# Kernel optimization log

Measured on AMD Instinct MI355X. Metric: run time of the kernel, lower is better.

Reference implementation:

```python
import jax, jax.numpy as jnp
import numpy as np
from jax.ops import segment_sum, segment_max

N, E, F, H, G, P, C = 50000, 600000, 128, 128, 64, 32, 10
HEADS = 3
BN_EPS = 1e-5
COS_EPS = 1e-8


def setup_inputs() -> dict:
    key = jax.random.key(0)
    ks = jax.random.split(key, 32)
    rn = lambda k, shape, s: jax.random.normal(k, shape, jnp.float32) * s
    inp = {
        "x": jax.random.normal(ks[0], (N, F), jnp.float32),
        "edge_index": jax.random.randint(ks[1], (2, E), 0, N, jnp.int32),
        "batch": jnp.sort(jax.random.randint(ks[2], (N,), 0, G, jnp.int32)),
        # GCNConv
        "W1": rn(ks[3], (F, H), F ** -0.5), "b1": jnp.zeros((H,), jnp.float32),
        # SAGEConv (lin_l on aggregated neighbors, lin_r on root)
        "Wl": rn(ks[4], (H, H), H ** -0.5), "Wr": rn(ks[5], (H, H), H ** -0.5),
        "bs": jnp.zeros((H,), jnp.float32),
        # GATConv, heads=3, concat=False
        "Wg": rn(ks[6], (H, HEADS * H), H ** -0.5),
        "a_src": rn(ks[7], (HEADS, H), H ** -0.5),
        "a_dst": rn(ks[8], (HEADS, H), H ** -0.5),
        "bg": jnp.zeros((H,), jnp.float32),
        # prototype head / classifier / decoder
        "protos": jax.random.normal(ks[9], (P, H), jnp.float32),
        "Wc": rn(ks[10], (H, C), H ** -0.5), "bc": jnp.zeros((C,), jnp.float32),
        "Wd1": rn(ks[11], (H, 2 * H), H ** -0.5), "bd1": jnp.zeros((2 * H,), jnp.float32),
        "Wd2": rn(ks[12], (2 * H, F), (2 * H) ** -0.5), "bd2": jnp.zeros((F,), jnp.float32),
    }
    # BatchNorm (eval mode): gamma, beta, running mean/var for bn1..bn3
    for i in range(3):
        k0, k1, k2 = jax.random.split(ks[13 + i], 3)
        inp[f"g{i+1}"] = 1.0 + rn(k0, (H,), 0.05)
        inp[f"be{i+1}"] = rn(k1, (H,), 0.05)
        inp[f"m{i+1}"] = rn(k2, (H,), 0.1)
        inp[f"v{i+1}"] = jnp.ones((H,), jnp.float32)
    return inp


def _bn(x, g, b, m, v):
    return (x - m) * jax.lax.rsqrt(v + BN_EPS) * g + b


def _forward(x, edge_index, batch,
             W1, b1, g1, be1, m1, v1,
             Wl, Wr, bs, g2, be2, m2, v2,
             Wg, a_src, a_dst, bg, g3, be3, m3, v3,
             protos, Wc, bc, Wd1, bd1, Wd2, bd2):
    src, dst = edge_index[0], edge_index[1]
    ones_e = jnp.ones((src.shape[0],), x.dtype)

    # --- GCNConv: symmetric norm with self-loops ---
    h = x @ W1                                        # [N, H]
    deg = segment_sum(ones_e, dst, num_segments=N) + 1.0
    dinv = jax.lax.rsqrt(deg)
    coef = dinv[src] * dinv[dst]                      # [E]
    h1 = segment_sum(h[src] * coef[:, None], dst, num_segments=N)
    h1 = h1 + h * (dinv * dinv)[:, None] + b1         # self-loop term + bias
    h1 = jax.nn.elu(_bn(h1, g1, be1, m1, v1))         # dropout = identity (eval)

    # --- SAGEConv: mean aggregation (no self-loops) ---
    cnt = segment_sum(ones_e, dst, num_segments=N)
    mean_nb = segment_sum(h1[src], dst, num_segments=N) / jnp.maximum(cnt, 1.0)[:, None]
    h2 = mean_nb @ Wl + h1 @ Wr + bs
    h2 = jax.nn.elu(_bn(h2, g2, be2, m2, v2))

    # --- GATConv: heads=3, concat=False (mean), with self-loops ---
    hg = (h2 @ Wg).reshape(N, HEADS, H)               # [N, 3, H]
    al_src = jnp.einsum('nhf,hf->nh', hg, a_src)      # [N, 3]
    al_dst = jnp.einsum('nhf,hf->nh', hg, a_dst)
    loop = jnp.arange(N, dtype=src.dtype)
    s2 = jnp.concatenate([src, loop])
    d2 = jnp.concatenate([dst, loop])
    e = jax.nn.leaky_relu(al_src[s2] + al_dst[d2], 0.2)   # [E+N, 3]
    emax = segment_max(e, d2, num_segments=N)             # every node has a self-loop
    ex = jnp.exp(e - emax[d2])
    den = segment_sum(ex, d2, num_segments=N)
    alpha = ex / den[d2]                                  # [E+N, 3]
    h3 = segment_sum(hg[s2] * alpha[:, :, None], d2, num_segments=N)
    h3 = h3.mean(axis=1) + bg                             # concat=False -> head mean
    h3 = jax.nn.elu(_bn(h3, g3, be3, m3, v3))

    # --- global mean pool over graphs ---
    gcnt = segment_sum(jnp.ones((N,), x.dtype), batch, num_segments=G)
    pooled = segment_sum(h3, batch, num_segments=G) / jnp.maximum(gcnt, 1.0)[:, None]

    # --- prototype head: cosine sim -> softmax -> mix ---
    xn = pooled / jnp.maximum(jnp.linalg.norm(pooled, axis=-1, keepdims=True), COS_EPS)
    pn = protos / jnp.maximum(jnp.linalg.norm(protos, axis=-1, keepdims=True), COS_EPS)
    sims = xn @ pn.T                                      # [G, P]
    assignments = jax.nn.softmax(sims, axis=-1)
    proto_emb = assignments @ protos                      # [G, H]
    logits = proto_emb @ Wc + bc                          # [G, C]
    reconstructed = jax.nn.relu(pooled @ Wd1 + bd1) @ Wd2 + bd2   # [G, F]
    return logits, proto_emb, assignments, reconstructed


def reference(x, edge_index, batch,
              W1, b1, g1, be1, m1, v1,
              Wl, Wr, bs, g2, be2, m2, v2,
              Wg, a_src, a_dst, bg, g3, be3, m3, v3,
              protos, Wc, bc, Wd1, bd1, Wd2, bd2):
    return _forward(x, edge_index, batch,
                    W1, b1, g1, be1, m1, v1,
                    Wl, Wr, bs, g2, be2, m2, v2,
                    Wg, a_src, a_dst, bg, g3, be3, m3, v3,
                    protos, Wc, bc, Wd1, bd1, Wd2, bd2)
```

## Files before the change

### kernel.cpp

```cpp
#include <hip/hip_runtime.h>
#include <hip/hip_bf16.h>
#include <stdint.h>
#include <stddef.h>

#define N_ 50000
#define E_ 600000
#define F_ 128
#define H_ 128
#define G_ 64
#define P_ 32
#define C_ 10
#define NB_ 49

typedef __hip_bfloat16 bf16;
typedef __attribute__((ext_vector_type(8))) short short8;
typedef __attribute__((ext_vector_type(4))) float float4v;

struct __align__(4) u3 { unsigned int x, y, z; };

__device__ __forceinline__ float b2f(bf16 x){ return __bfloat162float(x); }
__device__ __forceinline__ float us2f(unsigned short u){ return __uint_as_float(((unsigned int)u)<<16); }
__device__ __forceinline__ unsigned short f2us(float x){ bf16 h = __float2bfloat16(x); return *(unsigned short*)&h; }
__device__ __forceinline__ float blo(unsigned int u){ return __uint_as_float(u<<16); }
__device__ __forceinline__ float bhi(unsigned int u){ return __uint_as_float(u & 0xFFFF0000u); }
__device__ __forceinline__ float eluf(float x){ return x>0.f ? x : expm1f(x); }
__device__ __forceinline__ float bnf(float x,float m,float v,float g,float b){ return (x-m)*rsqrtf(v+1e-5f)*g+b; }
__device__ __forceinline__ float lrelu(float x){ return x>0.f ? x : 0.2f*x; }
__device__ __forceinline__ float expc(float x){ return __expf(fminf(x, 50.f)); }
__device__ __forceinline__ void atomAddF(float* a, float v){ unsafeAtomicAdd(a, v); }

__global__ __launch_bounds__(256) void k_wprep(const float* __restrict__ W1, const float* __restrict__ Wl,
    const float* __restrict__ Wr, const float* __restrict__ Wg, unsigned short* __restrict__ WT){
  int idx = blockIdx.x*256 + threadIdx.x;
  if(idx >= 6*16384) return;
  int m = idx >> 14, rem = idx & 16383;
  int n = rem >> 7, k = rem & 127;
  float v;
  if(m==0)      v = W1[k*128+n];
  else if(m==1) v = Wl[k*128+n];
  else if(m==2) v = Wr[k*128+n];
  else          v = Wg[k*384 + (m-3)*128 + n];
  WT[idx] = f2us(v);
}

__device__ __forceinline__ void stage_WT(const unsigned short* __restrict__ WTg, unsigned short* lds, int tid){
  #pragma unroll
  for(int i=0;i<8;i++){
    int idx = tid + i*256;
    int n = idx>>4, c = idx&15;
    uint4 v = *(const uint4*)(WTg + (size_t)idx*8);
    int cs = c ^ (n & 15);
    *(uint4*)(lds + n*128 + cs*8) = v;
  }
}
__device__ __forceinline__ short8 read_Bfrag(const unsigned short* lds, int tile, int kc, int lane){
  int n = tile*16 + (lane&15);
  int c = kc*4 + (lane>>4);
  int cs = c ^ (lane & 15);
  return *(const short8*)(lds + n*128 + cs*8);
}
__device__ __forceinline__ void load_Afrag_bf16(const bf16* A, int row, int lane, short8 af[4]){
  const unsigned short* ap = (const unsigned short*)A + (size_t)row*128 + (lane>>4)*8;
  #pragma unroll
  for(int kc=0;kc<4;kc++) af[kc] = *(const short8*)(ap + kc*32);
}
__device__ __forceinline__ void mfma_pass(const unsigned short* lds, const short8 af[4], int lane, float4v acc[8]){
  #pragma unroll
  for(int tile=0;tile<8;tile++){
    #pragma unroll
    for(int kc=0;kc<4;kc++){
      short8 bfv = read_Bfrag(lds, tile, kc, lane);
      acc[tile] = __builtin_amdgcn_mfma_f32_16x16x32_bf16(af[kc], bfv, acc[tile], 0, 0, 0);
    }
  }
}

__global__ __launch_bounds__(256) void k_mm_x(const float* __restrict__ X, const unsigned short* __restrict__ WTg,
                                              bf16* __restrict__ HB){
  __shared__ unsigned short Wlds[128*128];
  const int tid = threadIdx.x, lane = tid&63, w = tid>>6;
  const int row0 = blockIdx.x*64;
  stage_WT(WTg, Wlds, tid);
  int arow = row0 + w*16 + (lane&15);
  int ar = arow < N_ ? arow : N_-1;
  const float* ap = X + (size_t)ar*128 + (lane>>4)*8;
  short8 af[4];
  #pragma unroll
  for(int kc=0;kc<4;kc++){
    float4 a = *(const float4*)(ap + kc*32);
    float4 b = *(const float4*)(ap + kc*32 + 4);
    short8 v;
    v[0]=(short)f2us(a.x); v[1]=(short)f2us(a.y); v[2]=(short)f2us(a.z); v[3]=(short)f2us(a.w);
    v[4]=(short)f2us(b.x); v[5]=(short)f2us(b.y); v[6]=(short)f2us(b.z); v[7]=(short)f2us(b.w);
    af[kc]=v;
  }
  __syncthreads();
  float4v acc[8];
  #pragma unroll
  for(int t=0;t<8;t++){ acc[t][0]=0.f; acc[t][1]=0.f; acc[t][2]=0.f; acc[t][3]=0.f; }
  mfma_pass(Wlds, af, lane, acc);
  const int colb = lane&15, q = lane>>4;
  unsigned short* ob = (unsigned short*)HB;
  #pragma unroll
  for(int r=0;r<4;r++){
    int ro = row0 + w*16 + q*4 + r;
    if(ro < N_){
      #pragma unroll
      for(int tile=0;tile<8;tile++)
        ob[(size_t)ro*128 + tile*16 + colb] = f2us(acc[tile][r]);
    }
  }
}

__global__ __launch_bounds__(256) void k_sage_mm(const bf16* __restrict__ MaB, const bf16* __restrict__ H1B,
    const unsigned short* __restrict__ WlT, const unsigned short* __restrict__ WrT,
    const float* __restrict__ bs, const float* __restrict__ g2, const float* __restrict__ be2,
    const float* __restrict__ m2, const float* __restrict__ v2, bf16* __restrict__ H2B){
  __shared__ unsigned short Wlds[128*128];
  const int tid = threadIdx.x, lane = tid&63, w = tid>>6;
  const int row0 = blockIdx.x*64;
  int arow = row0 + w*16 + (lane&15);
  int ar = arow < N_ ? arow : N_-1;
  float4v acc[8];
  #pragma unroll
  for(int t=0;t<8;t++){ acc[t][0]=0.f; acc[t][1]=0.f; acc[t][2]=0.f; acc[t][3]=0.f; }
  short8 af[4];

  stage_WT(WlT, Wlds, tid);
  load_Afrag_bf16(MaB, ar, lane, af);
  __syncthreads();
  mfma_pass(Wlds, af, lane, acc);
  __syncthreads();
  stage_WT(WrT, Wlds, tid);
  load_Afrag_bf16(H1B, ar, lane, af);
  __syncthreads();
  mfma_pass(Wlds, af, lane, acc);

  const int colb = lane&15, q = lane>>4;
  unsigned short* ob = (unsigned short*)H2B;
  #pragma unroll
  for(int tile=0;tile<8;tile++){
    int col = tile*16 + colb;
    float bsv=bs[col], gv=g2[col], bev=be2[col], mv=m2[col], vv=v2[col];
    #pragma unroll
    for(int r=0;r<4;r++){
      int ro = row0 + w*16 + q*4 + r;
      if(ro < N_){
        float x = acc[tile][r] + bsv;
        ob[(size_t)ro*128 + col] = f2us(eluf(bnf(x, mv, vv, gv, bev)));
      }
    }
  }
}

__global__ __launch_bounds__(256) void k_gat_mm_all(const bf16* __restrict__ H2B, const unsigned short* __restrict__ WgT,
    const float* __restrict__ a_src, const float* __restrict__ a_dst,
    bf16* __restrict__ HG3I, float* __restrict__ als3, float* __restrict__ ald3){
  __shared__ unsigned short Wlds[128*128];
  const int tid = threadIdx.x, lane = tid&63, w = tid>>6;
  const int row0 = blockIdx.x*64;
  int arow = row0 + w*16 + (lane&15);
  int ar = arow < N_ ? arow : N_-1;
  short8 af[4];
  load_Afrag_bf16(H2B, ar, lane, af);
  const int colb = lane&15, q = lane>>4;
  unsigned short* ob = (unsigned short*)HG3I;
  for(int hh=0; hh<3; hh++){
    if(hh) __syncthreads();
    stage_WT(WgT + hh*16384, Wlds, tid);
    __syncthreads();
    float4v acc[8];
    #pragma unroll
    for(int t=0;t<8;t++){ acc[t][0]=0.f; acc[t][1]=0.f; acc[t][2]=0.f; acc[t][3]=0.f; }
    mfma_pass(Wlds, af, lane, acc);
    float asv[8], adv[8];
    #pragma unroll
    for(int tile=0;tile<8;tile++){
      asv[tile] = a_src[hh*128 + tile*16 + colb];
      adv[tile] = a_dst[hh*128 + tile*16 + colb];
    }
    #pragma unroll
    for(int r=0;r<4;r++){
      int ro = row0 + w*16 + q*4 + r;
      float ps = 0.f, pd = 0.f;
      #pragma unroll
      for(int tile=0;tile<8;tile++){ ps += acc[tile][r]*asv[tile]; pd += acc[tile][r]*adv[tile]; }
      #pragma unroll
      for(int o=8;o>0;o>>=1){ ps += __shfl_down(ps,o,16); pd += __shfl_down(pd,o,16); }
      if(ro < N_){
        #pragma unroll
        for(int tile=0;tile<8;tile++)
          ob[(size_t)ro*384 + (size_t)(tile*8 + (colb>>1))*6 + hh*2 + (colb&1)] = f2us(acc[tile][r]);
        if(colb == 0){ als3[ro*3+hh] = ps; ald3[ro*3+hh] = pd; }
      }
    }
  }
}

__global__ __launch_bounds__(256) void k_count(const int* __restrict__ dst, int* __restrict__ cnt){
  int e = blockIdx.x*256 + threadIdx.x;
  if(e < E_) atomicAdd(&cnt[dst[e]], 1);
}

__global__ __launch_bounds__(1024) void k_scan1(const int* __restrict__ cnt, int* __restrict__ row_ptr,
                                                float* __restrict__ dinv, int* __restrict__ bsum){
  __shared__ int wsum[16];
  const int t = threadIdx.x, lane = t & 63, wid = t >> 6;
  int i = blockIdx.x*1024 + t;
  int v = (i<N_) ? cnt[i] : 0;
  int x = v;
  #pragma unroll
  for(int o=1;o<64;o<<=1){
    int y = __shfl_up(x, o, 64);
    if(lane >= o) x += y;
  }
  if(lane==63) wsum[wid] = x;
  __syncthreads();
  if(wid==0){
    int s = (lane<16) ? wsum[lane] : 0;
    #pragma unroll
    for(int o=1;o<16;o<<=1){
      int y = __shfl_up(s, o, 64);
      if(lane >= o) s += y;
    }
    if(lane<16) wsum[lane] = s;
  }
  __syncthreads();
  int waveoff = (wid>0) ? wsum[wid-1] : 0;
  int incl = waveoff + x;
  if(i<N_){
    row_ptr[i] = incl - v;
    dinv[i] = rsqrtf((float)v + 1.f);
  }
  if(t==1023) bsum[blockIdx.x] = incl;
}

__global__ __launch_bounds__(64) void k_scan2(const int* __restrict__ bsum, int* __restrict__ boff,
                                              int* __restrict__ row_ptr){
  int lane = threadIdx.x;
  int v = (lane < NB_) ? bsum[lane] : 0;
  int x = v;
  #pragma unroll
  for(int o=1;o<64;o<<=1){
    int y = __shfl_up(x, o, 64);
    if(lane >= o) x += y;
  }
  if(lane < NB_) boff[lane] = x - v;
  if(lane == 63) row_ptr[N_] = x;
}

__global__ __launch_bounds__(256) void k_scan3(int* __restrict__ row_ptr, const int* __restrict__ boff,
                                               int* __restrict__ tmp){
  int i = blockIdx.x*256 + threadIdx.x;
  if(i < N_){
    int r = row_ptr[i] + boff[i>>10];
    row_ptr[i] = r;
    tmp[i] = r;
  }
}

__global__ __launch_bounds__(256) void k_scatter(const int* __restrict__ src, const int* __restrict__ dst,
                                                 int* __restrict__ tmp, int* __restrict__ esrc,
                                                 int* __restrict__ edst){
  int e = blockIdx.x*256 + threadIdx.x;
  if(e < E_){
    int d = dst[e];
    int pos = atomicAdd(&tmp[d], 1);
    esrc[pos] = src[e];
    edst[pos] = d;
  }
}

__global__ __launch_bounds__(256) void k_wexp(const int* __restrict__ esrc, const int* __restrict__ edst,
    const float* __restrict__ als3, const float* __restrict__ ald3, float* __restrict__ we4){
  int e = blockIdx.x*256 + threadIdx.x;
  if(e >= E_) return;
  int s = esrc[e], d = edst[e];
  float4 w;
  w.x = expc(lrelu(als3[s*3+0] + ald3[d*3+0]));
  w.y = expc(lrelu(als3[s*3+1] + ald3[d*3+1]));
  w.z = expc(lrelu(als3[s*3+2] + ald3[d*3+2]));
  w.w = 0.f;
  *(float4*)(we4 + (size_t)e*4) = w;
}

__global__ __launch_bounds__(256) void k_gcn_gather(const int* __restrict__ row_ptr, const int* __restrict__ esrc,
    const float* __restrict__ dinv, const bf16* __restrict__ HB,
    const float* __restrict__ b1, const float* __restrict__ g1, const float* __restrict__ be1,
    const float* __restrict__ m1, const float* __restrict__ v1, bf16* __restrict__ H1B){
  int n = blockIdx.x*4 + (threadIdx.x>>6);
  int lane = threadIdx.x & 63;
  if(n >= N_) return;
  int beg = row_ptr[n], end = row_ptr[n+1];
  float dn = dinv[n];
  float a0 = 0.f, a1 = 0.f;
  const unsigned short* hb = (const unsigned short*)HB;
  int e = beg;
  for(; e+3 < end; e += 4){
    int s0 = esrc[e], s1 = esrc[e+1], s2 = esrc[e+2], s3 = esrc[e+3];
    unsigned int hv0 = *(const unsigned int*)(hb + (size_t)s0*H_ + lane*2);
    unsigned int hv1 = *(const unsigned int*)(hb + (size_t)s1*H_ + lane*2);
    unsigned int hv2 = *(const unsigned int*)(hb + (size_t)s2*H_ + lane*2);
    unsigned int hv3 = *(const unsigned int*)(hb + (size_t)s3*H_ + lane*2);
    float c0 = dinv[s0]*dn, c1 = dinv[s1]*dn, c2 = dinv[s2]*dn, c3 = dinv[s3]*dn;
    a0 += c0*blo(hv0) + c1*blo(hv1) + c2*blo(hv2) + c3*blo(hv3);
    a1 += c0*bhi(hv0) + c1*bhi(hv1) + c2*bhi(hv2) + c3*bhi(hv3);
  }
  for(; e < end; e++){
    int s = esrc[e];
    float c = dinv[s]*dn;
    unsigned int hv = *(const unsigned int*)(hb + (size_t)s*H_ + lane*2);
    a0 += c*blo(hv);
    a1 += c*bhi(hv);
  }
  unsigned int hv = *(const unsigned int*)(hb + (size_t)n*H_ + lane*2);
  int f0 = lane*2, f1 = f0+1;
  float x0 = a0 + blo(hv)*dn*dn + b1[f0];
  float x1 = a1 + bhi(hv)*dn*dn + b1[f1];
  x0 = eluf(bnf(x0, m1[f0], v1[f0], g1[f0], be1[f0]));
  x1 = eluf(bnf(x1, m1[f1], v1[f1], g1[f1], be1[f1]));
  unsigned int o = ((unsigned int)f2us(x1)<<16) | f2us(x0);
  *(unsigned int*)((unsigned short*)H1B + (size_t)n*H_ + lane*2) = o;
}

__global__ __launch_bounds__(256) void k_sage_gather(const int* __restrict__ row_ptr, const int* __restrict__ esrc,
    const bf16* __restrict__ H1B, bf16* __restrict__ MeanB){
  int n = blockIdx.x*4 + (threadIdx.x>>6);
  int lane = threadIdx.x & 63;
  if(n >= N_) return;
  int beg = row_ptr[n], end = row_ptr[n+1];
  float a0 = 0.f, a1 = 0.f;
  const unsigned short* hb = (const unsigned short*)H1B;
  int e = beg;
  for(; e+3 < end; e += 4){
    int s0 = esrc[e], s1 = esrc[e+1], s2 = esrc[e+2], s3 = esrc[e+3];
    unsigned int hv0 = *(const unsigned int*)(hb + (size_t)s0*H_ + lane*2);
    unsigned int hv1 = *(const unsigned int*)(hb + (size_t)s1*H_ + lane*2);
    unsigned int hv2 = *(const unsigned int*)(hb + (size_t)s2*H_ + lane*2);
    unsigned int hv3 = *(const unsigned int*)(hb + (size_t)s3*H_ + lane*2);
    a0 += blo(hv0) + blo(hv1) + blo(hv2) + blo(hv3);
    a1 += bhi(hv0) + bhi(hv1) + bhi(hv2) + bhi(hv3);
  }
  for(; e < end; e++){
    unsigned int hv = *(const unsigned int*)(hb + (size_t)esrc[e]*H_ + lane*2);
    a0 += blo(hv);
    a1 += bhi(hv);
  }
  float inv = 1.f / fmaxf((float)(end-beg), 1.f);
  unsigned int o = ((unsigned int)f2us(a1*inv)<<16) | f2us(a0*inv);
  *(unsigned int*)((unsigned short*)MeanB + (size_t)n*H_ + lane*2) = o;
}

__global__ __launch_bounds__(256) void k_gat_gather3(const int* __restrict__ row_ptr, const int* __restrict__ esrc,
    const float* __restrict__ als3, const float* __restrict__ ald3, const float* __restrict__ we4,
    const bf16* __restrict__ HG3I, bf16* __restrict__ H3B){
  int n = blockIdx.x*4 + (threadIdx.x>>6);
  int lane = threadIdx.x & 63;
  if(n >= N_) return;
  int beg = row_ptr[n], end = row_ptr[n+1];
  float es0 = expc(lrelu(als3[n*3+0] + ald3[n*3+0]));
  float es1 = expc(lrelu(als3[n*3+1] + ald3[n*3+1]));
  float es2 = expc(lrelu(als3[n*3+2] + ald3[n*3+2]));
  const unsigned short* hb = (const unsigned short*)HG3I;
  const int lp6 = lane*6;
  u3 hs = *(const u3*)(hb + (size_t)n*384 + lp6);
  float den0 = es0, den1 = es1, den2 = es2;
  float a00 = es0*blo(hs.x), a01 = es0*bhi(hs.x);
  float a10 = es1*blo(hs.y), a11 = es1*bhi(hs.y);
  float a20 = es2*blo(hs.z), a21 = es2*bhi(hs.z);
  int e = beg;
  for(; e+3 < end; e += 4){
    int s0 = esrc[e], s1 = esrc[e+1], s2 = esrc[e+2], s3 = esrc[e+3];
    float4 w0 = *(const float4*)(we4 + (size_t)(e  )*4);
    float4 w1 = *(const float4*)(we4 + (size_t)(e+1)*4);
    float4 w2 = *(const float4*)(we4 + (size_t)(e+2)*4);
    float4 w3 = *(const float4*)(we4 + (size_t)(e+3)*4);
    u3 p0 = *(const u3*)(hb + (size_t)s0*384 + lp6);
    u3 p1 = *(const u3*)(hb + (size_t)s1*384 + lp6);
    u3 p2 = *(const u3*)(hb + (size_t)s2*384 + lp6);
    u3 p3 = *(const u3*)(hb + (size_t)s3*384 + lp6);
    den0 += w0.x + w1.x + w2.x + w3.x;
    den1 += w0.y + w1.y + w2.y + w3.y;
    den2 += w0.z + w1.z + w2.z + w3.z;
    a00 += w0.x*blo(p0.x) + w1.x*blo(p1.x) + w2.x*blo(p2.x) + w3.x*blo(p3.x);
    a01 += w0.x*bhi(p0.x) + w1.x*bhi(p1.x) + w2.x*bhi(p2.x) + w3.x*bhi(p3.x);
    a10 += w0.y*blo(p0.y) + w1.y*blo(p1.y) + w2.y*blo(p2.y) + w3.y*blo(p3.y);
    a11 += w0.y*bhi(p0.y) + w1.y*bhi(p1.y) + w2.y*bhi(p2.y) + w3.y*bhi(p3.y);
    a20 += w0.z*blo(p0.z) + w1.z*blo(p1.z) + w2.z*blo(p2.z) + w3.z*blo(p3.z);
    a21 += w0.z*bhi(p0.z) + w1.z*bhi(p1.z) + w2.z*bhi(p2.z) + w3.z*bhi(p3.z);
  }
  for(; e < end; e++){
    int s = esrc[e];
    float4 w = *(const float4*)(we4 + (size_t)e*4);
    u3 p = *(const u3*)(hb + (size_t)s*384 + lp6);
    den0 += w.x; den1 += w.y; den2 += w.z;
    a00 += w.x*blo(p.x); a01 += w.x*bhi(p.x);
    a10 += w.y*blo(p.y); a11 += w.y*bhi(p.y);
    a20 += w.z*blo(p.z); a21 += w.z*bhi(p.z);
  }
  float i0 = 1.f/(3.f*den0), i1 = 1.f/(3.f*den1), i2 = 1.f/(3.f*den2);
  float r0 = a00*i0 + a10*i1 + a20*i2;
  float r1 = a01*i0 + a11*i1 + a21*i2;
  unsigned int o = ((unsigned int)f2us(r1)<<16) | f2us(r0);
  *(unsigned int*)((unsigned short*)H3B + (size_t)n*H_ + lane*2) = o;
}

#define NPW_ 16
__global__ __launch_bounds__(256) void k_h3fin_pool(const bf16* __restrict__ ACCB, const float* __restrict__ bg,
    const float* __restrict__ g3, const float* __restrict__ be3, const float* __restrict__ m3, const float* __restrict__ v3,
    const int* __restrict__ batch, float* __restrict__ pooled, float* __restrict__ gcnt){
  int wave = blockIdx.x*4 + (threadIdx.x>>6);
  int lane = threadIdx.x & 63;
  int n0 = wave*NPW_;
  if(n0 >= N_) return;
  int n1 = n0 + NPW_; if(n1 > N_) n1 = N_;
  int f0 = lane*2, f1 = f0+1;
  float bg0=bg[f0], bg1=bg[f1];
  float g30=g3[f0], g31=g3[f1], be30=be3[f0], be31=be3[f1];
  float m30=m3[f0], m31=m3[f1], v30=v3[f0], v31=v3[f1];
  float r0=0.f, r1=0.f;
  int cur = batch[n0];
  int seg = 0;
  for(int n=n0; n<n1; n++){
    int b = batch[n];
    if(b != cur){
      atomAddF(&pooled[cur*H_ + f0], r0);
      atomAddF(&pooled[cur*H_ + f1], r1);
      if(lane==0) atomAddF(&gcnt[cur], (float)seg);
      r0 = 0.f; r1 = 0.f; seg = 0; cur = b;
    }
    unsigned int hv = *(const unsigned int*)((const unsigned short*)ACCB + (size_t)n*H_ + lane*2);
    float x0 = blo(hv) + bg0;
    float x1 = bhi(hv) + bg1;
    r0 += eluf(bnf(x0, m30, v30, g30, be30));
    r1 += eluf(bnf(x1, m31, v31, g31, be31));
    seg++;
  }
  atomAddF(&pooled[cur*H_ + f0], r0);
  atomAddF(&pooled[cur*H_ + f1], r1);
  if(lane==0) atomAddF(&gcnt[cur], (float)seg);
}

__global__ __launch_bounds__(128) void k_head(const float* __restrict__ pooledacc, const float* __restrict__ gcnt,
    const float* __restrict__ protos, const float* __restrict__ Wc, const float* __restrict__ bc,
    const float* __restrict__ Wd1, const float* __restrict__ bd1, const float* __restrict__ Wd2, const float* __restrict__ bd2,
    float* __restrict__ out){
  const int g = blockIdx.x, t = threadIdx.x;
  __shared__ float p[128], xn[128], red[128], sims[32], es[32], asg[32], pe[128], t1[256];
  __shared__ float nrm;
  float cg_ = fmaxf(gcnt[g], 1.f);
  p[t] = pooledacc[g*128 + t] / cg_;
  __syncthreads();
  red[t] = p[t]*p[t];
  __syncthreads();
  for(int s=64;s>0;s>>=1){ if(t<s) red[t]+=red[t+s]; __syncthreads(); }
  if(t==0) nrm = fmaxf(sqrtf(red[0]), 1e-8f);
  __syncthreads();
  xn[t] = p[t]/nrm;
  __syncthreads();
  if(t<32){
    float s=0.f, pn=0.f;
    for(int f=0;f<128;f++){ float pv=protos[t*128+f]; s += xn[f]*pv; pn += pv*pv; }
    sims[t] = s / fmaxf(sqrtf(pn), 1e-8f);
  }
  __syncthreads();
  if(t<32){
    float mx=-1e30f;
    for(int j=0;j<32;j++) mx = fmaxf(mx, sims[j]);
    es[t] = __expf(sims[t]-mx);
  }
  __syncthreads();
  if(t<32){
    float sm=0.f;
    for(int j=0;j<32;j++) sm += es[j];
    float a = es[t]/fmaxf(sm,1e-20f);
    asg[t] = a;
    out[8832 + g*32 + t] = a;
  }
  __syncthreads();
  {
    float s=0.f;
    for(int pp=0;pp<32;pp++) s += asg[pp]*protos[pp*128+t];
    pe[t] = s;
    out[640 + g*128 + t] = s;
  }
  __syncthreads();
  if(t<10){
    float s = bc[t];
    for(int f=0;f<128;f++) s += pe[f]*Wc[f*10+t];
    out[g*10 + t] = s;
  }
  for(int j=t;j<256;j+=128){
    float s = bd1[j];
    for(int f=0;f<128;f++) s += p[f]*Wd1[f*256+j];
    t1[j] = fmaxf(s, 0.f);
  }
  __syncthreads();
  {
    float s = bd2[t];
    for(int j=0;j<256;j++) s += t1[j]*Wd2[j*128+t];
    out[10880 + g*128 + t] = s;
  }
}

__global__ void k_sentinel(float* out, float code){
  out[0] = code;
}

extern "C" void kernel_launch(void* const* d_in, const int* in_sizes, int n_in,
                              void* d_out, int out_size, void* d_ws, size_t ws_size,
                              hipStream_t stream){
  const float* X    = (const float*)d_in[0];
  const int*  EI    = (const int*)d_in[1];
  const int*  batch = (const int*)d_in[2];
  const int* src = EI;
  const int* dst = EI + E_;

  int iW1,ib1,iWl,iWr,ibs,iWg,ias,iad,ibg,ipr,iWc,ibc,iWd1,ibd1,iWd2,ibd2;
  int ig1,ibe1,im1,iv1,ig2,ibe2,im2,iv2,ig3,ibe3,im3,iv3;
  if(n_in >= 31 && in_sizes[5] == 128){
    iW1=3; ib1=4; ig1=5; ibe1=6; im1=7; iv1=8;
    iWl=9; iWr=10; ibs=11; ig2=12; ibe2=13; im2=14; iv2=15;
    iWg=16; ias=17; iad=18; ibg=19; ig3=20; ibe3=21; im3=22; iv3=23;
    ipr=24; iWc=25; ibc=26; iWd1=27; ibd1=28; iWd2=29; ibd2=30;
  }else{
    iW1=3; ib1=4; iWl=5; iWr=6; ibs=7; iWg=8; ias=9; iad=10; ibg=11;
    ipr=12; iWc=13; ibc=14; iWd1=15; ibd1=16; iWd2=17; ibd2=18;
    ig1=19; ibe1=20; im1=21; iv1=22; ig2=23; ibe2=24; im2=25; iv2=26;
    ig3=27; ibe3=28; im3=29; iv3=30;
  }
  const float* W1 = (const float*)d_in[iW1];   const float* b1 = (const float*)d_in[ib1];
  const float* Wl = (const float*)d_in[iWl];   const float* Wr = (const float*)d_in[iWr];
  const float* bs = (const float*)d_in[ibs];   const float* Wg = (const float*)d_in[iWg];
  const float* a_src = (const float*)d_in[ias]; const float* a_dst = (const float*)d_in[iad];
  const float* bg = (const float*)d_in[ibg];   const float* protos = (const float*)d_in[ipr];
  const float* Wc = (const float*)d_in[iWc];   const float* bc = (const float*)d_in[ibc];
  const float* Wd1 = (const float*)d_in[iWd1]; const float* bd1 = (const float*)d_in[ibd1];
  const float* Wd2 = (const float*)d_in[iWd2]; const float* bd2 = (const float*)d_in[ibd2];
  const float* g1 = (const float*)d_in[ig1];   const float* be1 = (const float*)d_in[ibe1];
  const float* m1 = (const float*)d_in[im1];   const float* v1 = (const float*)d_in[iv1];
  const float* g2 = (const float*)d_in[ig2];   const float* be2 = (const float*)d_in[ibe2];
  const float* m2 = (const float*)d_in[im2];   const float* v2 = (const float*)d_in[iv2];
  const float* g3 = (const float*)d_in[ig3];   const float* be3 = (const float*)d_in[ibe3];
  const float* m3 = (const float*)d_in[im3];   const float* v3 = (const float*)d_in[iv3];

  const size_t NF = (size_t)N_*H_;
  const size_t intN = (size_t)3*N_ + 4 + (size_t)2*E_ + 128;
  const size_t fltN = (size_t)7*N_ + (size_t)4*E_ + G_*H_ + G_;
  const size_t NEED = NF*2*3 + (size_t)N_*384*2 + intN*4 + fltN*4 + (size_t)6*16384*2;
  if(ws_size < NEED){
    k_sentinel<<<1,1,0,stream>>>((float*)d_out, 1000.f + (float)(ws_size>>20));
    return;
  }
  bf16* RA = (bf16*)d_ws;
  bf16* RB = RA + NF;
  bf16* RC = RB + NF;
  bf16* HG3 = RC + NF;
  int*  cnt     = (int*)(HG3 + (size_t)N_*384);
  int*  row_ptr = cnt + N_;
  int*  tmp     = row_ptr + (N_+4);
  int*  esrc    = tmp + N_;
  int*  edst    = esrc + E_;
  int*  bsum    = edst + E_;
  int*  boff    = bsum + 64;
  float* dinv   = (float*)(boff + 64);
  float* als3   = dinv + N_;
  float* ald3   = als3 + (size_t)N_*3;
  float* we4    = ald3 + (size_t)N_*3;
  float* pooled = we4 + (size_t)E_*4;
  float* gcnt   = pooled + (size_t)G_*H_;
  unsigned short* WTg = (unsigned short*)(gcnt + G_);

  k_wprep<<<(6*16384+255)/256, 256, 0, stream>>>(W1, Wl, Wr, Wg, WTg);
  hipMemsetAsync(cnt, 0, N_*sizeof(int), stream);
  k_count<<<(E_+255)/256, 256, 0, stream>>>(dst, cnt);
  k_scan1<<<NB_, 1024, 0, stream>>>(cnt, row_ptr, dinv, bsum);
  k_scan2<<<1, 64, 0, stream>>>(bsum, boff, row_ptr);
  k_scan3<<<(N_+255)/256, 256, 0, stream>>>(row_ptr, boff, tmp);
  k_scatter<<<(E_+255)/256, 256, 0, stream>>>(src, dst, tmp, esrc, edst);

  const int GB = (N_+3)/4;
  const int MB = (N_+63)/64;
  k_mm_x<<<MB, 256, 0, stream>>>(X, WTg, RA);
  k_gcn_gather<<<GB, 256, 0, stream>>>(row_ptr, esrc, dinv, RA, b1, g1, be1, m1, v1, RB);
  k_sage_gather<<<GB, 256, 0, stream>>>(row_ptr, esrc, RB, RC);
  k_sage_mm<<<MB, 256, 0, stream>>>(RC, RB, WTg + 16384, WTg + 2*16384, bs, g2, be2, m2, v2, RA);
  k_gat_mm_all<<<MB, 256, 0, stream>>>(RA, WTg + 3*16384, a_src, a_dst, HG3, als3, ald3);
  k_wexp<<<(E_+255)/256, 256, 0, stream>>>(esrc, edst, als3, ald3, we4);
  k_gat_gather3<<<GB, 256, 0, stream>>>(row_ptr, esrc, als3, ald3, we4, HG3, RC);
  hipMemsetAsync(pooled, 0, (size_t)(G_*H_+G_)*sizeof(float), stream);
  {
    int waves = (N_ + NPW_ - 1)/NPW_;
    int blocks = (waves + 3)/4;
    k_h3fin_pool<<<blocks, 256, 0, stream>>>(RC, bg, g3, be3, m3, v3, batch, pooled, gcnt);
  }
  k_head<<<G_, 128, 0, stream>>>(pooled, gcnt, protos, Wc, bc, Wd1, bd1, Wd2, bd2, (float*)d_out);
}
```

Measured before the change: 452.4 us.

## Reorder GAT to aggregate H2 before projection and fold attention vectors into weights

Attention logits are now computed as dot products of H2 with precomputed Wg·a_src and Wg·a_dst vectors, fused into the SAGE matmul epilogue. GAT aggregation now gathers 128-wide H2 rows instead of 384-wide projected rows and writes per-head aggregates U. A single K=384 matmul then applies Wg and the BN/ELU epilogue. The goal is to cut gather traffic in the edge-heavy aggregation by about a factor of three, at the cost of an extra matmul pass over a 384-wide intermediate and different bf16 rounding order.

```diff
diff --git a/kernel.cpp b/kernel.cpp
--- a/kernel.cpp
+++ b/kernel.cpp
@@ -16,13 +16,11 @@
 typedef __attribute__((ext_vector_type(8))) short short8;
 typedef __attribute__((ext_vector_type(4))) float float4v;
 
-struct __align__(4) u3 { unsigned int x, y, z; };
-
-__device__ __forceinline__ float b2f(bf16 x){ return __bfloat162float(x); }
 __device__ __forceinline__ float us2f(unsigned short u){ return __uint_as_float(((unsigned int)u)<<16); }
 __device__ __forceinline__ unsigned short f2us(float x){ bf16 h = __float2bfloat16(x); return *(unsigned short*)&h; }
 __device__ __forceinline__ float blo(unsigned int u){ return __uint_as_float(u<<16); }
 __device__ __forceinline__ float bhi(unsigned int u){ return __uint_as_float(u & 0xFFFF0000u); }
+__device__ __forceinline__ unsigned int packbf(float lo, float hi){ return ((unsigned int)f2us(hi)<<16) | f2us(lo); }
 __device__ __forceinline__ float eluf(float x){ return x>0.f ? x : expm1f(x); }
 __device__ __forceinline__ float bnf(float x,float m,float v,float g,float b){ return (x-m)*rsqrtf(v+1e-5f)*g+b; }
 __device__ __forceinline__ float lrelu(float x){ return x>0.f ? x : 0.2f*x; }
@@ -43,6 +41,24 @@
   WT[idx] = f2us(v);
 }
 
+__global__ __launch_bounds__(384) void k_vprep(const float* __restrict__ Wg, const float* __restrict__ a_src,
+    const float* __restrict__ a_dst, float* __restrict__ vs3, float* __restrict__ vd3){
+  int t = threadIdx.x;
+  if(t >= 384) return;
+  int h = t >> 7, f = t & 127;
+  const float4* wr = (const float4*)(Wg + (size_t)f*384 + h*128);
+  const float4* as = (const float4*)(a_src + h*128);
+  const float4* ad = (const float4*)(a_dst + h*128);
+  float s = 0.f, d = 0.f;
+  #pragma unroll 8
+  for(int j=0;j<32;j++){
+    float4 wv = wr[j], av = as[j], dv = ad[j];
+    s += wv.x*av.x + wv.y*av.y + wv.z*av.z + wv.w*av.w;
+    d += wv.x*dv.x + wv.y*dv.y + wv.z*dv.z + wv.w*dv.w;
+  }
+  vs3[t] = s; vd3[t] = d;
+}
+
 __device__ __forceinline__ void stage_WT(const unsigned short* __restrict__ WTg, unsigned short* lds, int tid){
   #pragma unroll
   for(int i=0;i<8;i++){
@@ -112,10 +128,12 @@
   }
 }
 
-__global__ __launch_bounds__(256) void k_sage_mm(const bf16* __restrict__ MaB, const bf16* __restrict__ H1B,
+__global__ __launch_bounds__(256) void k_sage_mm_att(const bf16* __restrict__ MaB, const bf16* __restrict__ H1B,
     const unsigned short* __restrict__ WlT, const unsigned short* __restrict__ WrT,
     const float* __restrict__ bs, const float* __restrict__ g2, const float* __restrict__ be2,
-    const float* __restrict__ m2, const float* __restrict__ v2, bf16* __restrict__ H2B){
+    const float* __restrict__ m2, const float* __restrict__ v2,
+    const float* __restrict__ vs3, const float* __restrict__ vd3,
+    bf16* __restrict__ H2B, float* __restrict__ als3, float* __restrict__ ald3){
   __shared__ unsigned short Wlds[128*128];
   const int tid = threadIdx.x, lane = tid&63, w = tid>>6;
   const int row0 = blockIdx.x*64;
@@ -137,6 +155,15 @@
   mfma_pass(Wlds, af, lane, acc);
 
   const int colb = lane&15, q = lane>>4;
+  float vsv[24], vdv[24];
+  #pragma unroll
+  for(int h=0;h<3;h++){
+    #pragma unroll
+    for(int tile=0;tile<8;tile++){
+      vsv[h*8+tile] = vs3[h*128 + tile*16 + colb];
+      vdv[h*8+tile] = vd3[h*128 + tile*16 + colb];
+    }
+  }
   unsigned short* ob = (unsigned short*)H2B;
   #pragma unroll
   for(int tile=0;tile<8;tile++){
@@ -145,53 +172,59 @@
     #pragma unroll
     for(int r=0;r<4;r++){
       int ro = row0 + w*16 + q*4 + r;
-      if(ro < N_){
-        float x = acc[tile][r] + bsv;
-        ob[(size_t)ro*128 + col] = f2us(eluf(bnf(x, mv, vv, gv, bev)));
-      }
-    }
-  }
-}
-
-__global__ __launch_bounds__(256) void k_gat_mm_all(const bf16* __restrict__ H2B, const unsigned short* __restrict__ WgT,
-    const float* __restrict__ a_src, const float* __restrict__ a_dst,
-    bf16* __restrict__ HG3I, float* __restrict__ als3, float* __restrict__ ald3){
+      float x = eluf(bnf(acc[tile][r] + bsv, mv, vv, gv, bev));
+      acc[tile][r] = x;
+      if(ro < N_) ob[(size_t)ro*128 + col] = f2us(x);
+    }
+  }
+  #pragma unroll
+  for(int r=0;r<4;r++){
+    int ro = row0 + w*16 + q*4 + r;
+    #pragma unroll
+    for(int h=0;h<3;h++){
+      float ps=0.f, pd=0.f;
+      #pragma unroll
+      for(int tile=0;tile<8;tile++){ ps += acc[tile][r]*vsv[h*8+tile]; pd += acc[tile][r]*vdv[h*8+tile]; }
+      #pragma unroll
+      for(int o=8;o>0;o>>=1){ ps += __shfl_down(ps,o,16); pd += __shfl_down(pd,o,16); }
+      if(colb==0 && ro<N_){ als3[ro*3+h] = ps; ald3[ro*3+h] = pd; }
+    }
+  }
+}
+
+__global__ __launch_bounds__(256) void k_gat_mm3(const bf16* __restrict__ U, const unsigned short* __restrict__ WgT,
+    const float* __restrict__ bg, const float* __restrict__ g3, const float* __restrict__ be3,
+    const float* __restrict__ m3, const float* __restrict__ v3, bf16* __restrict__ H3B){
   __shared__ unsigned short Wlds[128*128];
   const int tid = threadIdx.x, lane = tid&63, w = tid>>6;
   const int row0 = blockIdx.x*64;
   int arow = row0 + w*16 + (lane&15);
   int ar = arow < N_ ? arow : N_-1;
+  float4v acc[8];
+  #pragma unroll
+  for(int t=0;t<8;t++){ acc[t][0]=0.f; acc[t][1]=0.f; acc[t][2]=0.f; acc[t][3]=0.f; }
   short8 af[4];
-  load_Afrag_bf16(H2B, ar, lane, af);
-  const int colb = lane&15, q = lane>>4;
-  unsigned short* ob = (unsigned short*)HG3I;
   for(int hh=0; hh<3; hh++){
     if(hh) __syncthreads();
     stage_WT(WgT + hh*16384, Wlds, tid);
+    const unsigned short* ap = (const unsigned short*)U + (size_t)ar*384 + hh*128 + (lane>>4)*8;
+    #pragma unroll
+    for(int kc=0;kc<4;kc++) af[kc] = *(const short8*)(ap + kc*32);
     __syncthreads();
-    float4v acc[8];
-    #pragma unroll
-    for(int t=0;t<8;t++){ acc[t][0]=0.f; acc[t][1]=0.f; acc[t][2]=0.f; acc[t][3]=0.f; }
     mfma_pass(Wlds, af, lane, acc);
-    float asv[8], adv[8];
-    #pragma unroll
-    for(int tile=0;tile<8;tile++){
-      asv[tile] = a_src[hh*128 + tile*16 + colb];
-      adv[tile] = a_dst[hh*128 + tile*16 + colb];
-    }
+  }
+  const int colb = lane&15, q = lane>>4;
+  unsigned short* ob = (unsigned short*)H3B;
+  #pragma unroll
+  for(int tile=0;tile<8;tile++){
+    int col = tile*16 + colb;
+    float bgv=bg[col], gv=g3[col], bev=be3[col], mv=m3[col], vv=v3[col];
     #pragma unroll
     for(int r=0;r<4;r++){
       int ro = row0 + w*16 + q*4 + r;
-      float ps = 0.f, pd = 0.f;
-      #pragma unroll
-      for(int tile=0;tile<8;tile++){ ps += acc[tile][r]*asv[tile]; pd += acc[tile][r]*adv[tile]; }
-      #pragma unroll
-      for(int o=8;o>0;o>>=1){ ps += __shfl_down(ps,o,16); pd += __shfl_down(pd,o,16); }
       if(ro < N_){
-        #pragma unroll
-        for(int tile=0;tile<8;tile++)
-          ob[(size_t)ro*384 + (size_t)(tile*8 + (colb>>1))*6 + hh*2 + (colb&1)] = f2us(acc[tile][r]);
-        if(colb == 0){ als3[ro*3+hh] = ps; ald3[ro*3+hh] = pd; }
+        float x = acc[tile][r] + bgv;
+        ob[(size_t)ro*128 + col] = f2us(eluf(bnf(x, mv, vv, gv, bev)));
       }
     }
   }
@@ -351,9 +384,9 @@
   *(unsigned int*)((unsigned short*)MeanB + (size_t)n*H_ + lane*2) = o;
 }
 
-__global__ __launch_bounds__(256) void k_gat_gather3(const int* __restrict__ row_ptr, const int* __restrict__ esrc,
+__global__ __launch_bounds__(256) void k_gat_agg(const int* __restrict__ row_ptr, const int* __restrict__ esrc,
     const float* __restrict__ als3, const float* __restrict__ ald3, const float* __restrict__ we4,
-    const bf16* __restrict__ HG3I, bf16* __restrict__ H3B){
+    const bf16* __restrict__ H2B, bf16* __restrict__ U){
   int n = blockIdx.x*4 + (threadIdx.x>>6);
   int lane = threadIdx.x & 63;
   if(n >= N_) return;
@@ -361,13 +394,13 @@
   float es0 = expc(lrelu(als3[n*3+0] + ald3[n*3+0]));
   float es1 = expc(lrelu(als3[n*3+1] + ald3[n*3+1]));
   float es2 = expc(lrelu(als3[n*3+2] + ald3[n*3+2]));
-  const unsigned short* hb = (const unsigned short*)HG3I;
-  const int lp6 = lane*6;
-  u3 hs = *(const u3*)(hb + (size_t)n*384 + lp6);
+  const unsigned short* hb = (const unsigned short*)H2B;
+  unsigned int xs = *(const unsigned int*)(hb + (size_t)n*H_ + lane*2);
+  float x0 = blo(xs), x1 = bhi(xs);
   float den0 = es0, den1 = es1, den2 = es2;
-  float a00 = es0*blo(hs.x), a01 = es0*bhi(hs.x);
-  float a10 = es1*blo(hs.y), a11 = es1*bhi(hs.y);
-  float a20 = es2*blo(hs.z), a21 = es2*bhi(hs.z);
+  float a00 = es0*x0, a01 = es0*x1;
+  float a10 = es1*x0, a11 = es1*x1;
+  float a20 = es2*x0, a21 = es2*x1;
   int e = beg;
   for(; e+3 < end; e += 4){
     int s0 = esrc[e], s1 = esrc[e+1], s2 = esrc[e+2], s3 = esrc[e+3];
@@ -375,39 +408,42 @@
     float4 w1 = *(const float4*)(we4 + (size_t)(e+1)*4);
     float4 w2 = *(const float4*)(we4 + (size_t)(e+2)*4);
     float4 w3 = *(const float4*)(we4 + (size_t)(e+3)*4);
-    u3 p0 = *(const u3*)(hb + (size_t)s0*384 + lp6);
-    u3 p1 = *(const u3*)(hb + (size_t)s1*384 + lp6);
-    u3 p2 = *(const u3*)(hb + (size_t)s2*384 + lp6);
-    u3 p3 = *(const u3*)(hb + (size_t)s3*384 + lp6);
+    unsigned int p0 = *(const unsigned int*)(hb + (size_t)s0*H_ + lane*2);
+    unsigned int p1 = *(const unsigned int*)(hb + (size_t)s1*H_ + lane*2);
+    unsigned int p2 = *(const unsigned int*)(hb + (size_t)s2*H_ + lane*2);
+    unsigned int p3 = *(const unsigned int*)(hb + (size_t)s3*H_ + lane*2);
     den0 += w0.x + w1.x + w2.x + w3.x;
     den1 += w0.y + w1.y + w2.y + w3.y;
     den2 += w0.z + w1.z + w2.z + w3.z;
-    a00 += w0.x*blo(p0.x) + w1.x*blo(p1.x) + w2.x*blo(p2.x) + w3.x*blo(p3.x);
-    a01 += w0.x*bhi(p0.x) + w1.x*bhi(p1.x) + w2.x*bhi(p2.x) + w3.x*bhi(p3.x);
-    a10 += w0.y*blo(p0.y) + w1.y*blo(p1.y) + w2.y*blo(p2.y) + w3.y*blo(p3.y);
-    a11 += w0.y*bhi(p0.y) + w1.y*bhi(p1.y) + w2.y*bhi(p2.y) + w3.y*bhi(p3.y);
-    a20 += w0.z*blo(p0.z) + w1.z*blo(p1.z) + w2.z*blo(p2.z) + w3.z*blo(p3.z);
-    a21 += w0.z*bhi(p0.z) + w1.z*bhi(p1.z) + w2.z*bhi(p2.z) + w3.z*bhi(p3.z);
+    float q00=blo(p0), q01=bhi(p0), q10=blo(p1), q11=bhi(p1);
+    float q20=blo(p2), q21=bhi(p2), q30=blo(p3), q31=bhi(p3);
+    a00 += w0.x*q00 + w1.x*q10 + w2.x*q20 + w3.x*q30;
+    a01 += w0.x*q01 + w1.x*q11 + w2.x*q21 + w3.x*q31;
+    a10 += w0.y*q00 + w1.y*q10 + w2.y*q20 + w3.y*q30;
+    a11 += w0.y*q01 + w1.y*q11 + w2.y*q21 + w3.y*q31;
+    a20 += w0.z*q00 + w1.z*q10 + w2.z*q20 + w3.z*q30;
+    a21 += w0.z*q01 + w1.z*q11 + w2.z*q21 + w3.z*q31;
   }
   for(; e < end; e++){
     int s = esrc[e];
     float4 w = *(const float4*)(we4 + (size_t)e*4);
-    u3 p = *(const u3*)(hb + (size_t)s*384 + lp6);
+    unsigned int p = *(const unsigned int*)(hb + (size_t)s*H_ + lane*2);
+    float q0 = blo(p), q1 = bhi(p);
     den0 += w.x; den1 += w.y; den2 += w.z;
-    a00 += w.x*blo(p.x); a01 += w.x*bhi(p.x);
-    a10 += w.y*blo(p.y); a11 += w.y*bhi(p.y);
-    a20 += w.z*blo(p.z); a21 += w.z*bhi(p.z);
+    a00 += w.x*q0; a01 += w.x*q1;
+    a10 += w.y*q0; a11 += w.y*q1;
+    a20 += w.z*q0; a21 += w.z*q1;
   }
   float i0 = 1.f/(3.f*den0), i1 = 1.f/(3.f*den1), i2 = 1.f/(3.f*den2);
-  float r0 = a00*i0 + a10*i1 + a20*i2;
-  float r1 = a01*i0 + a11*i1 + a21*i2;
-  unsigned int o = ((unsigned int)f2us(r1)<<16) | f2us(r0);
-  *(unsigned int*)((unsigned short*)H3B + (size_t)n*H_ + lane*2) = o;
+  unsigned short* ub = (unsigned short*)U;
+  size_t ubase = (size_t)n*384 + lane*2;
+  *(unsigned int*)(ub + ubase)       = packbf(a00*i0, a01*i0);
+  *(unsigned int*)(ub + ubase + 128) = packbf(a10*i1, a11*i1);
+  *(unsigned int*)(ub + ubase + 256) = packbf(a20*i2, a21*i2);
 }
 
 #define NPW_ 16
-__global__ __launch_bounds__(256) void k_h3fin_pool(const bf16* __restrict__ ACCB, const float* __restrict__ bg,
-    const float* __restrict__ g3, const float* __restrict__ be3, const float* __restrict__ m3, const float* __restrict__ v3,
+__global__ __launch_bounds__(256) void k_h3pool(const bf16* __restrict__ H3B,
     const int* __restrict__ batch, float* __restrict__ pooled, float* __restrict__ gcnt){
   int wave = blockIdx.x*4 + (threadIdx.x>>6);
   int lane = threadIdx.x & 63;
@@ -415,9 +451,6 @@
   if(n0 >= N_) return;
   int n1 = n0 + NPW_; if(n1 > N_) n1 = N_;
   int f0 = lane*2, f1 = f0+1;
-  float bg0=bg[f0], bg1=bg[f1];
-  float g30=g3[f0], g31=g3[f1], be30=be3[f0], be31=be3[f1];
-  float m30=m3[f0], m31=m3[f1], v30=v3[f0], v31=v3[f1];
   float r0=0.f, r1=0.f;
   int cur = batch[n0];
   int seg = 0;
@@ -429,11 +462,9 @@
       if(lane==0) atomAddF(&gcnt[cur], (float)seg);
       r0 = 0.f; r1 = 0.f; seg = 0; cur = b;
     }
-    unsigned int hv = *(const unsigned int*)((const unsigned short*)ACCB + (size_t)n*H_ + lane*2);
-    float x0 = blo(hv) + bg0;
-    float x1 = bhi(hv) + bg1;
-    r0 += eluf(bnf(x0, m30, v30, g30, be30));
-    r1 += eluf(bnf(x1, m31, v31, g31, be31));
+    unsigned int hv = *(const unsigned int*)((const unsigned short*)H3B + (size_t)n*H_ + lane*2);
+    r0 += blo(hv);
+    r1 += bhi(hv);
     seg++;
   }
   atomAddF(&pooled[cur*H_ + f0], r0);
@@ -546,7 +577,7 @@
 
   const size_t NF = (size_t)N_*H_;
   const size_t intN = (size_t)3*N_ + 4 + (size_t)2*E_ + 128;
-  const size_t fltN = (size_t)7*N_ + (size_t)4*E_ + G_*H_ + G_;
+  const size_t fltN = (size_t)7*N_ + (size_t)4*E_ + G_*H_ + G_ + 768;
   const size_t NEED = NF*2*3 + (size_t)N_*384*2 + intN*4 + fltN*4 + (size_t)6*16384*2;
   if(ws_size < NEED){
     k_sentinel<<<1,1,0,stream>>>((float*)d_out, 1000.f + (float)(ws_size>>20));
@@ -555,8 +586,8 @@
   bf16* RA = (bf16*)d_ws;
   bf16* RB = RA + NF;
   bf16* RC = RB + NF;
-  bf16* HG3 = RC + NF;
-  int*  cnt     = (int*)(HG3 + (size_t)N_*384);
+  bf16* U  = RC + NF;
+  int*  cnt     = (int*)(U + (size_t)N_*384);
   int*  row_ptr = cnt + N_;
   int*  tmp     = row_ptr + (N_+4);
   int*  esrc    = tmp + N_;
@@ -569,9 +600,12 @@
   float* we4    = ald3 + (size_t)N_*3;
   float* pooled = we4 + (size_t)E_*4;
   float* gcnt   = pooled + (size_t)G_*H_;
-  unsigned short* WTg = (unsigned short*)(gcnt + G_);
+  float* vs3    = gcnt + G_;
+  float* vd3    = vs3 + 384;
+  unsigned short* WTg = (unsigned short*)(vd3 + 384);
 
   k_wprep<<<(6*16384+255)/256, 256, 0, stream>>>(W1, Wl, Wr, Wg, WTg);
+  k_vprep<<<1, 384, 0, stream>>>(Wg, a_src, a_dst, vs3, vd3);
   hipMemsetAsync(cnt, 0, N_*sizeof(int), stream);
   k_count<<<(E_+255)/256, 256, 0, stream>>>(dst, cnt);
   k_scan1<<<NB_, 1024, 0, stream>>>(cnt, row_ptr, dinv, bsum);
@@ -584,15 +618,16 @@
   k_mm_x<<<MB, 256, 0, stream>>>(X, WTg, RA);
   k_gcn_gather<<<GB, 256, 0, stream>>>(row_ptr, esrc, dinv, RA, b1, g1, be1, m1, v1, RB);
   k_sage_gather<<<GB, 256, 0, stream>>>(row_ptr, esrc, RB, RC);
-  k_sage_mm<<<MB, 256, 0, stream>>>(RC, RB, WTg + 16384, WTg + 2*16384, bs, g2, be2, m2, v2, RA);
-  k_gat_mm_all<<<MB, 256, 0, stream>>>(RA, WTg + 3*16384, a_src, a_dst, HG3, als3, ald3);
+  k_sage_mm_att<<<MB, 256, 0, stream>>>(RC, RB, WTg + 16384, WTg + 2*16384, bs, g2, be2, m2, v2,
+                                        vs3, vd3, RA, als3, ald3);
   k_wexp<<<(E_+255)/256, 256, 0, stream>>>(esrc, edst, als3, ald3, we4);
-  k_gat_gather3<<<GB, 256, 0, stream>>>(row_ptr, esrc, als3, ald3, we4, HG3, RC);
+  k_gat_agg<<<GB, 256, 0, stream>>>(row_ptr, esrc, als3, ald3, we4, RA, U);
+  k_gat_mm3<<<MB, 256, 0, stream>>>(U, WTg + 3*16384, bg, g3, be3, m3, v3, RC);
   hipMemsetAsync(pooled, 0, (size_t)(G_*H_+G_)*sizeof(float), stream);
   {
     int waves = (N_ + NPW_ - 1)/NPW_;
     int blocks = (waves + 3)/4;
-    k_h3fin_pool<<<blocks, 256, 0, stream>>>(RC, bg, g3, be3, m3, v3, batch, pooled, gcnt);
+    k_h3pool<<<blocks, 256, 0, stream>>>(RC, batch, pooled, gcnt);
   }
   k_head<<<G_, 128, 0, stream>>>(pooled, gcnt, protos, Wc, bc, Wd1, bd1, Wd2, bd2, (float*)d_out);
 }
```

After: 438.0 us. -3.2%, faster.
